# Kernel optimization log

Hardware: AMD Instinct MI355X
Metric: run time of the kernel (lower is better)

The kernel has to match this reference:

```python
import jax, jax.numpy as jnp
import numpy as np

B, LQ, LK, C = 16, 1024, 1024, 512
WH = int(LQ ** 0.5)  # 32


def setup_inputs() -> dict:
    key = jax.random.key(0)
    ks = jax.random.split(key, 6)
    s1 = 1.0 / np.sqrt(LK)
    return {
        "query": jax.random.normal(ks[0], (B, LQ, C), jnp.float32),
        "key": jax.random.normal(ks[1], (B, LK, C), jnp.float32),
        "value": jax.random.normal(ks[2], (B, LK, C), jnp.float32),
        # nn.Linear weights, stored [out_features, in_features] like torch
        "w1": jax.random.normal(ks[3], (LK, LK), jnp.float32) * s1,
        "w2": jax.random.normal(ks[4], (LK, LK), jnp.float32) * s1,
        "w3": jax.random.normal(ks[5], (1, LK), jnp.float32) * s1,
    }


def reference(query, key, value, w1, w2, w3):
    # cosine-similarity matrix (computed under no_grad in the original)
    q = query / 100.0
    k = key / 100.0
    qn = jnp.sqrt(jnp.sum(q * q, axis=-1))[:, :, None]   # [B, LQ, 1]
    kn = jnp.sqrt(jnp.sum(k * k, axis=-1))[:, None, :]   # [B, 1, LK]
    outer = qn * kn                                       # rank-1 outer product [B, LQ, LK]
    upper = jnp.einsum('bqc,bkc->bqk', q, k)              # [B, LQ, LK]
    similar_rev = jax.lax.stop_gradient(upper / (outer + 1e-6))

    # 3-layer MLP gating over the LK axis -> scalar weight per query row
    h = jax.nn.gelu(jnp.einsum('bqk,ok->bqo', similar_rev, w1), approximate=False)
    h = jax.nn.gelu(jnp.einsum('bqk,ok->bqo', h, w2), approximate=False)
    w = jnp.einsum('bqk,ok->bqo', h, w3)[..., 0]          # [B, LQ]

    # weight^T @ similar_rev / wh, then tanh -> per-key scalar gate [B, LK, 1]
    weight = jnp.einsum('bq,bqk->bk', w, similar_rev) / WH
    weight = jnp.tanh(weight)[:, :, None]

    # value modulation + residual
    return value * weight + value
```

## Files before the change

kernel.cpp:

```cpp
#include <hip/hip_runtime.h>
#include <hip/hip_bf16.h>

#define B_  16
#define LQ_ 1024
#define LK_ 1024
#define C_  512

typedef __attribute__((ext_vector_type(4))) float f32x4;
typedef __attribute__((ext_vector_type(8))) short bf16x8;

__device__ __forceinline__ float bf2f(ushort u) {
  union { unsigned int i; float f; } v; v.i = ((unsigned int)u) << 16; return v.f;
}
__device__ __forceinline__ ushort f2bf(float f) {
  union { float f; unsigned int i; } v; v.f = f;
  unsigned int r = v.i + 0x7fffu + ((v.i >> 16) & 1u);
  return (ushort)(r >> 16);
}
__device__ __forceinline__ float gelu_fast(float x) {
  float u = x * (0.7978845608f + 0.0356774081f * x * x);
  u = fminf(fmaxf(u, -9.f), 9.f);
  float e = __expf(2.f * u);
  float t = (e - 1.f) / (e + 1.f);
  return 0.5f * x * (1.f + t);
}

__device__ __forceinline__ void gload_lds16(const ushort* g, ushort* l) {
  __builtin_amdgcn_global_load_lds(
      (const __attribute__((address_space(1))) void*)g,
      (__attribute__((address_space(3))) void*)l, 16, 0, 0);
}

__global__ __launch_bounds__(256) void prep_all(
    const float* __restrict__ q, const float* __restrict__ k,
    const float* __restrict__ w1, const float* __restrict__ w2,
    ushort* __restrict__ Qb, ushort* __restrict__ Kb,
    ushort* __restrict__ W1b, ushort* __restrict__ W2b,
    float* __restrict__ qn, float* __restrict__ kn) {
  int wid = blockIdx.x * 4 + (threadIdx.x >> 6);
  int lane = threadIdx.x & 63;
  const float* src;
  ushort* dst;
  float* nrm = nullptr;
  if (wid < 16384) {
    src = q + (long)wid * C_;  dst = Qb + (long)wid * C_;  nrm = qn + wid;
  } else if (wid < 32768) {
    int r = wid - 16384;
    src = k + (long)r * C_;    dst = Kb + (long)r * C_;    nrm = kn + r;
  } else if (wid < 34816) {
    int r = wid - 32768;
    src = w1 + (long)r * C_;   dst = W1b + (long)r * C_;
  } else {
    int r = wid - 34816;
    src = w2 + (long)r * C_;   dst = W2b + (long)r * C_;
  }
  float ss = 0.f;
#pragma unroll
  for (int i0 = 0; i0 < 2; ++i0) {
    int i = lane * 4 + i0 * 256;
    float4 v = *(const float4*)(src + i);
    ss += v.x * v.x + v.y * v.y + v.z * v.z + v.w * v.w;
    ushort4 o;
    o.x = f2bf(v.x); o.y = f2bf(v.y); o.z = f2bf(v.z); o.w = f2bf(v.w);
    *(ushort4*)(dst + i) = o;
  }
  if (nrm) {
#pragma unroll
    for (int off = 32; off > 0; off >>= 1) ss += __shfl_xor(ss, off);
    if (lane == 0) *nrm = sqrtf(ss);
  }
}

#define BK 32

template <int EPI>
__device__ __forceinline__ void gemm128_body(
    const ushort* __restrict__ A, const ushort* __restrict__ Bm,
    ushort* __restrict__ Cc, int K, long sA, long sB, long sC,
    const float* __restrict__ qn, const float* __restrict__ kn,
    const float* __restrict__ w3v, float* __restrict__ wv) {
  int per = (int)(gridDim.x >> 3);
  int orig = blockIdx.x;
  int id = (orig & 7) * per + (orig >> 3);
  int b = id >> 6;
  int rtile = id & 63;
  const int bm = (rtile >> 3) * 128, bn = (rtile & 7) * 128;

  A += (long)b * sA;
  Bm += (long)b * sB;

  __shared__ ushort smem[16384];

  int tid = threadIdx.x;
  int lane = tid & 63, w = tid >> 6;
  int wr = w >> 1, wc = w & 1;
  int l16 = lane & 15, lhi = lane >> 4;

  f32x4 acc[4][4] = {};

  int c0 = tid, c1 = tid + 256;
  int r0 = c0 >> 2, cb0 = (c0 & 3) ^ ((r0 >> 1) & 3);
  int r1 = c1 >> 2, cb1 = (c1 & 3) ^ ((r1 >> 1) & 3);
  int wb0 = (tid & ~63) * 8;
  int wb1 = wb0 + 256 * 8;

  const ushort* Ar0 = A + (long)(bm + r0) * K + cb0 * 8;
  const ushort* Ar1 = A + (long)(bm + r1) * K + cb1 * 8;
  const ushort* Br0 = Bm + (long)(bn + r0) * K + cb0 * 8;
  const ushort* Br1 = Bm + (long)(bn + r1) * K + cb1 * 8;

  const int nt = K / BK;
  gload_lds16(Ar0, smem + wb0);
  gload_lds16(Ar1, smem + wb1);
  gload_lds16(Br0, smem + 8192 + wb0);
  gload_lds16(Br1, smem + 8192 + wb1);
  __syncthreads();

  int cur = 0;
  for (int t = 0; t < nt; ++t) {
    if (t + 1 < nt) {
      int k1 = (t + 1) * BK;
      int nx = (cur ^ 1) * 4096;
      gload_lds16(Ar0 + k1, smem + nx + wb0);
      gload_lds16(Ar1 + k1, smem + nx + wb1);
      gload_lds16(Br0 + k1, smem + 8192 + nx + wb0);
      gload_lds16(Br1 + k1, smem + 8192 + nx + wb1);
    }

    const ushort* Ac = smem + cur * 4096;
    const ushort* Bc = smem + 8192 + cur * 4096;
    bf16x8 af[4], bfr[4];
#pragma unroll
    for (int m = 0; m < 4; ++m) {
      int r = wr * 64 + m * 16 + l16;
      af[m] = *(const bf16x8*)(Ac + r * 32 + ((lhi ^ ((r >> 1) & 3)) * 8));
    }
#pragma unroll
    for (int n = 0; n < 4; ++n) {
      int r = wc * 64 + n * 16 + l16;
      bfr[n] = *(const bf16x8*)(Bc + r * 32 + ((lhi ^ ((r >> 1) & 3)) * 8));
    }
#pragma unroll
    for (int m = 0; m < 4; ++m)
#pragma unroll
      for (int n = 0; n < 4; ++n)
        acc[m][n] = __builtin_amdgcn_mfma_f32_16x16x32_bf16(af[m], bfr[n],
                                                            acc[m][n], 0, 0, 0);
    __syncthreads();
    cur ^= 1;
  }

  if constexpr (EPI == 2) {
    float* wvb = wv + (long)b * LQ_;
    float w3c[4];
#pragma unroll
    for (int n = 0; n < 4; ++n) w3c[n] = w3v[bn + wc * 64 + n * 16 + l16];
#pragma unroll
    for (int m = 0; m < 4; ++m)
#pragma unroll
      for (int rr = 0; rr < 4; ++rr) {
        float s = 0.f;
#pragma unroll
        for (int n = 0; n < 4; ++n)
          s += gelu_fast(acc[m][n][rr]) * w3c[n];
        s += __shfl_xor(s, 1);
        s += __shfl_xor(s, 2);
        s += __shfl_xor(s, 4);
        s += __shfl_xor(s, 8);
        if (l16 == 0)
          atomicAdd(&wvb[bm + wr * 64 + m * 16 + lhi * 4 + rr], s);
      }
  } else {
    Cc += (long)b * sC;
    const float* qnb = qn + (long)b * LQ_;
    const float* knb = kn + (long)b * LK_;
#pragma unroll
    for (int m = 0; m < 4; ++m) {
      int row0 = bm + wr * 64 + m * 16 + lhi * 4;
#pragma unroll
      for (int n = 0; n < 4; ++n) {
        int col = bn + wc * 64 + n * 16 + l16;
#pragma unroll
        for (int rr = 0; rr < 4; ++rr) {
          float v = acc[m][n][rr];
          int grow = row0 + rr;
          if (EPI == 0) {
            v = v / (qnb[grow] * knb[col] + 1e-2f);
          } else {
            v = gelu_fast(v);
          }
          Cc[(long)grow * 1024 + col] = f2bf(v);
        }
      }
    }
  }
}

__global__ __launch_bounds__(256, 2) void gemm_s(
    const ushort* __restrict__ A, const ushort* __restrict__ Bm,
    ushort* __restrict__ Cc, const float* __restrict__ qn,
    const float* __restrict__ kn) {
  gemm128_body<0>(A, Bm, Cc, C_, (long)LQ_ * C_, (long)LK_ * C_,
                  (long)LQ_ * LK_, qn, kn, nullptr, nullptr);
}

__global__ __launch_bounds__(256, 2) void gemm_h1(
    const ushort* __restrict__ A, const ushort* __restrict__ Bm,
    ushort* __restrict__ Cc) {
  gemm128_body<1>(A, Bm, Cc, LK_, (long)LQ_ * LK_, 0L, (long)LQ_ * LK_,
                  nullptr, nullptr, nullptr, nullptr);
}

__global__ __launch_bounds__(256, 2) void gemm_h2w(
    const ushort* __restrict__ A, const ushort* __restrict__ Bm,
    const float* __restrict__ w3v, float* __restrict__ wv) {
  gemm128_body<2>(A, Bm, nullptr, LK_, (long)LQ_ * LK_, 0L, 0L,
                  nullptr, nullptr, w3v, wv);
}

__global__ __launch_bounds__(256) void gate_partial(const ushort* __restrict__ S,
                                                    const float* __restrict__ wv,
                                                    float* __restrict__ wraw) {
  int b = blockIdx.z;
  int q0 = blockIdx.y * 64;
  int k4 = threadIdx.x * 4;
  const ushort* p = S + (long)b * LQ_ * LK_ + (long)q0 * LK_ + k4;
  const float* wb = wv + b * LQ_ + q0;
  float a0 = 0.f, a1 = 0.f, a2 = 0.f, a3 = 0.f;
#pragma unroll 4
  for (int q = 0; q < 64; ++q) {
    float wq = wb[q];
    ushort4 s4 = *(const ushort4*)(p + (long)q * LK_);
    a0 += wq * bf2f(s4.x);
    a1 += wq * bf2f(s4.y);
    a2 += wq * bf2f(s4.z);
    a3 += wq * bf2f(s4.w);
  }
  float* wr = wraw + b * LK_ + k4;
  atomicAdd(wr + 0, a0);
  atomicAdd(wr + 1, a1);
  atomicAdd(wr + 2, a2);
  atomicAdd(wr + 3, a3);
}

__global__ __launch_bounds__(256) void finalize(const float* __restrict__ value,
                                                const float* __restrict__ wraw,
                                                float* __restrict__ out) {
  long i = (long)blockIdx.x * 256 + threadIdx.x;
  long e = i * 4;
  int row = (int)(e >> 9);
  float g = 1.f + tanhf(wraw[row] * (1.f / 32.f));
  float4 v = ((const float4*)value)[i];
  v.x *= g; v.y *= g; v.z *= g; v.w *= g;
  ((float4*)out)[i] = v;
}

extern "C" void kernel_launch(void* const* d_in, const int* in_sizes, int n_in,
                              void* d_out, int out_size, void* d_ws,
                              size_t ws_size, hipStream_t stream) {
  const float* query = (const float*)d_in[0];
  const float* key   = (const float*)d_in[1];
  const float* value = (const float*)d_in[2];
  const float* w1    = (const float*)d_in[3];
  const float* w2    = (const float*)d_in[4];
  const float* w3    = (const float*)d_in[5];
  float* out = (float*)d_out;

  const size_t QB_BYTES = (size_t)B_ * LQ_ * C_ * 2;
  const size_t S_BYTES  = (size_t)B_ * LQ_ * LK_ * 2;
  const size_t W_BYTES  = (size_t)LK_ * LK_ * 2;
  const size_t OFF_QB = 0;
  const size_t OFF_KB = OFF_QB + QB_BYTES;
  const size_t OFF_S  = OFF_KB + QB_BYTES;
  const size_t OFF_H1 = OFF_S + S_BYTES;
  const size_t OFF_W1 = OFF_H1 + S_BYTES;
  const size_t OFF_W2 = OFF_W1 + W_BYTES;
  const size_t OFF_QN = OFF_W2 + W_BYTES;
  const size_t OFF_KN = OFF_QN + (size_t)B_ * LQ_ * 4;
  const size_t OFF_WV = OFF_KN + (size_t)B_ * LK_ * 4;
  const size_t OFF_WR = OFF_WV + (size_t)B_ * LQ_ * 4;
  const size_t TOTAL  = OFF_WR + (size_t)B_ * LK_ * 4;
  if (ws_size < TOTAL) return;

  char* ws = (char*)d_ws;
  ushort* Qb  = (ushort*)(ws + OFF_QB);
  ushort* Kb  = (ushort*)(ws + OFF_KB);
  ushort* S   = (ushort*)(ws + OFF_S);
  ushort* h1  = (ushort*)(ws + OFF_H1);
  ushort* W1b = (ushort*)(ws + OFF_W1);
  ushort* W2b = (ushort*)(ws + OFF_W2);
  float* qn   = (float*)(ws + OFF_QN);
  float* kn   = (float*)(ws + OFF_KN);
  float* wv   = (float*)(ws + OFF_WV);
  float* wraw = (float*)(ws + OFF_WR);

  prep_all<<<dim3(9216), 256, 0, stream>>>(query, key, w1, w2, Qb, Kb, W1b,
                                           W2b, qn, kn);
  hipMemsetAsync(wraw, 0, (size_t)B_ * LK_ * 4, stream);
  hipMemsetAsync(wv, 0, (size_t)B_ * LQ_ * 4, stream);

  gemm_s<<<dim3(1024), 256, 0, stream>>>(Qb, Kb, S, qn, kn);

  gemm_h1<<<dim3(1024), 256, 0, stream>>>(S, W1b, h1);

  gemm_h2w<<<dim3(1024), 256, 0, stream>>>(h1, W2b, w3, wv);

  gate_partial<<<dim3(1, 16, B_), 256, 0, stream>>>(S, wv, wraw);

  finalize<<<dim3((size_t)B_ * LK_ * C_ / 4 / 256), 256, 0, stream>>>(value, wraw, out);
}
```

Before: 171.3 us.

## Switch all GEMM operands and intermediates from bf16 to fp8 e4m3 MFMA

```diff
diff --git a/kernel.cpp b/kernel.cpp
--- a/kernel.cpp
+++ b/kernel.cpp
@@ -7,15 +7,10 @@
 #define C_  512
 
 typedef __attribute__((ext_vector_type(4))) float f32x4;
-typedef __attribute__((ext_vector_type(8))) short bf16x8;
+typedef unsigned char uchar;
 
 __device__ __forceinline__ float bf2f(ushort u) {
   union { unsigned int i; float f; } v; v.i = ((unsigned int)u) << 16; return v.f;
-}
-__device__ __forceinline__ ushort f2bf(float f) {
-  union { float f; unsigned int i; } v; v.f = f;
-  unsigned int r = v.i + 0x7fffu + ((v.i >> 16) & 1u);
-  return (ushort)(r >> 16);
 }
 __device__ __forceinline__ float gelu_fast(float x) {
   float u = x * (0.7978845608f + 0.0356774081f * x * x);
@@ -25,7 +20,31 @@
   return 0.5f * x * (1.f + t);
 }
 
-__device__ __forceinline__ void gload_lds16(const ushort* g, ushort* l) {
+__device__ __forceinline__ uchar f2fp8(float x) {
+  float ax = fabsf(x);
+  ax = fminf(ax, 448.f);
+  unsigned int sgn = (__float_as_uint(x) >> 24) & 0x80u;
+  unsigned int b;
+  if (ax >= 0.015625f) {
+    unsigned int u = __float_as_uint(ax);
+    u += 0x7FFFFu + ((u >> 20) & 1u);
+    unsigned int e = (u >> 23) - 120u;
+    b = (e << 3) | ((u >> 20) & 7u);
+  } else {
+    b = (unsigned int)(ax * 512.f + 0.5f);
+  }
+  return (uchar)(sgn | b);
+}
+__device__ __forceinline__ float fp82f(unsigned int b) {
+  unsigned int e = (b >> 3) & 15u, m = b & 7u;
+  unsigned int ee = e ? e : 1u;
+  unsigned int mm = m + (e ? 8u : 0u);
+  union { unsigned int u; float f; } p; p.u = (ee + 117u) << 23;
+  float r = (float)mm * p.f;
+  return (b & 0x80u) ? -r : r;
+}
+
+__device__ __forceinline__ void gload_lds16(const uchar* g, uchar* l) {
   __builtin_amdgcn_global_load_lds(
       (const __attribute__((address_space(1))) void*)g,
       (__attribute__((address_space(3))) void*)l, 16, 0, 0);
@@ -34,14 +53,15 @@
 __global__ __launch_bounds__(256) void prep_all(
     const float* __restrict__ q, const float* __restrict__ k,
     const float* __restrict__ w1, const float* __restrict__ w2,
-    ushort* __restrict__ Qb, ushort* __restrict__ Kb,
-    ushort* __restrict__ W1b, ushort* __restrict__ W2b,
+    uchar* __restrict__ Qb, uchar* __restrict__ Kb,
+    uchar* __restrict__ W1b, uchar* __restrict__ W2b,
     float* __restrict__ qn, float* __restrict__ kn) {
   int wid = blockIdx.x * 4 + (threadIdx.x >> 6);
   int lane = threadIdx.x & 63;
   const float* src;
-  ushort* dst;
+  uchar* dst;
   float* nrm = nullptr;
+  float scale = 1.f;
   if (wid < 16384) {
     src = q + (long)wid * C_;  dst = Qb + (long)wid * C_;  nrm = qn + wid;
   } else if (wid < 32768) {
@@ -49,10 +69,10 @@
     src = k + (long)r * C_;    dst = Kb + (long)r * C_;    nrm = kn + r;
   } else if (wid < 34816) {
     int r = wid - 32768;
-    src = w1 + (long)r * C_;   dst = W1b + (long)r * C_;
+    src = w1 + (long)r * C_;   dst = W1b + (long)r * C_;   scale = 32.f;
   } else {
     int r = wid - 34816;
-    src = w2 + (long)r * C_;   dst = W2b + (long)r * C_;
+    src = w2 + (long)r * C_;   dst = W2b + (long)r * C_;   scale = 32.f;
   }
   float ss = 0.f;
 #pragma unroll
@@ -60,9 +80,11 @@
     int i = lane * 4 + i0 * 256;
     float4 v = *(const float4*)(src + i);
     ss += v.x * v.x + v.y * v.y + v.z * v.z + v.w * v.w;
-    ushort4 o;
-    o.x = f2bf(v.x); o.y = f2bf(v.y); o.z = f2bf(v.z); o.w = f2bf(v.w);
-    *(ushort4*)(dst + i) = o;
+    unsigned int pk = (unsigned int)f2fp8(v.x * scale) |
+                      ((unsigned int)f2fp8(v.y * scale) << 8) |
+                      ((unsigned int)f2fp8(v.z * scale) << 16) |
+                      ((unsigned int)f2fp8(v.w * scale) << 24);
+    *(unsigned int*)(dst + i) = pk;
   }
   if (nrm) {
 #pragma unroll
@@ -75,8 +97,8 @@
 
 template <int EPI>
 __device__ __forceinline__ void gemm128_body(
-    const ushort* __restrict__ A, const ushort* __restrict__ Bm,
-    ushort* __restrict__ Cc, int K, long sA, long sB, long sC,
+    const uchar* __restrict__ A, const uchar* __restrict__ Bm,
+    uchar* __restrict__ Cc, int K, long sA, long sB, long sC,
     const float* __restrict__ qn, const float* __restrict__ kn,
     const float* __restrict__ w3v, float* __restrict__ wv) {
   int per = (int)(gridDim.x >> 3);
@@ -89,7 +111,7 @@
   A += (long)b * sA;
   Bm += (long)b * sB;
 
-  __shared__ ushort smem[16384];
+  __shared__ uchar smem[16384];
 
   int tid = threadIdx.x;
   int lane = tid & 63, w = tid >> 6;
@@ -98,22 +120,16 @@
 
   f32x4 acc[4][4] = {};
 
-  int c0 = tid, c1 = tid + 256;
-  int r0 = c0 >> 2, cb0 = (c0 & 3) ^ ((r0 >> 1) & 3);
-  int r1 = c1 >> 2, cb1 = (c1 & 3) ^ ((r1 >> 1) & 3);
-  int wb0 = (tid & ~63) * 8;
-  int wb1 = wb0 + 256 * 8;
-
-  const ushort* Ar0 = A + (long)(bm + r0) * K + cb0 * 8;
-  const ushort* Ar1 = A + (long)(bm + r1) * K + cb1 * 8;
-  const ushort* Br0 = Bm + (long)(bn + r0) * K + cb0 * 8;
-  const ushort* Br1 = Bm + (long)(bn + r1) * K + cb1 * 8;
+  int sr = tid >> 1;
+  int sh = (tid & 1) ^ (sr & 1);
+  int wb = (tid & ~63) * 16;
+
+  const uchar* Asrc = A + (long)(bm + sr) * K + sh * 16;
+  const uchar* Bsrc = Bm + (long)(bn + sr) * K + sh * 16;
 
   const int nt = K / BK;
-  gload_lds16(Ar0, smem + wb0);
-  gload_lds16(Ar1, smem + wb1);
-  gload_lds16(Br0, smem + 8192 + wb0);
-  gload_lds16(Br1, smem + 8192 + wb1);
+  gload_lds16(Asrc, smem + wb);
+  gload_lds16(Bsrc, smem + 8192 + wb);
   __syncthreads();
 
   int cur = 0;
@@ -121,31 +137,29 @@
     if (t + 1 < nt) {
       int k1 = (t + 1) * BK;
       int nx = (cur ^ 1) * 4096;
-      gload_lds16(Ar0 + k1, smem + nx + wb0);
-      gload_lds16(Ar1 + k1, smem + nx + wb1);
-      gload_lds16(Br0 + k1, smem + 8192 + nx + wb0);
-      gload_lds16(Br1 + k1, smem + 8192 + nx + wb1);
+      gload_lds16(Asrc + k1, smem + nx + wb);
+      gload_lds16(Bsrc + k1, smem + 8192 + nx + wb);
     }
 
-    const ushort* Ac = smem + cur * 4096;
-    const ushort* Bc = smem + 8192 + cur * 4096;
-    bf16x8 af[4], bfr[4];
+    const uchar* Ac = smem + cur * 4096;
+    const uchar* Bc = smem + 8192 + cur * 4096;
+    long af[4], bfr[4];
 #pragma unroll
     for (int m = 0; m < 4; ++m) {
       int r = wr * 64 + m * 16 + l16;
-      af[m] = *(const bf16x8*)(Ac + r * 32 + ((lhi ^ ((r >> 1) & 3)) * 8));
+      af[m] = *(const long*)(Ac + r * 32 + (((lhi >> 1) ^ (r & 1)) * 16 + (lhi & 1) * 8));
     }
 #pragma unroll
     for (int n = 0; n < 4; ++n) {
       int r = wc * 64 + n * 16 + l16;
-      bfr[n] = *(const bf16x8*)(Bc + r * 32 + ((lhi ^ ((r >> 1) & 3)) * 8));
+      bfr[n] = *(const long*)(Bc + r * 32 + (((lhi >> 1) ^ (r & 1)) * 16 + (lhi & 1) * 8));
     }
 #pragma unroll
     for (int m = 0; m < 4; ++m)
 #pragma unroll
       for (int n = 0; n < 4; ++n)
-        acc[m][n] = __builtin_amdgcn_mfma_f32_16x16x32_bf16(af[m], bfr[n],
-                                                            acc[m][n], 0, 0, 0);
+        acc[m][n] = __builtin_amdgcn_mfma_f32_16x16x32_fp8_fp8(
+            af[m], bfr[n], acc[m][n], 0, 0, 0);
     __syncthreads();
     cur ^= 1;
   }
@@ -162,7 +176,7 @@
         float s = 0.f;
 #pragma unroll
         for (int n = 0; n < 4; ++n)
-          s += gelu_fast(acc[m][n][rr]) * w3c[n];
+          s += gelu_fast(acc[m][n][rr] * (1.f / 512.f)) * w3c[n];
         s += __shfl_xor(s, 1);
         s += __shfl_xor(s, 2);
         s += __shfl_xor(s, 4);
@@ -187,9 +201,9 @@
           if (EPI == 0) {
             v = v / (qnb[grow] * knb[col] + 1e-2f);
           } else {
-            v = gelu_fast(v);
+            v = gelu_fast(v * (1.f / 512.f));
           }
-          Cc[(long)grow * 1024 + col] = f2bf(v);
+          Cc[(long)grow * 1024 + col] = f2fp8(v * 16.f);
         }
       }
     }
@@ -197,44 +211,44 @@
 }
 
 __global__ __launch_bounds__(256, 2) void gemm_s(
-    const ushort* __restrict__ A, const ushort* __restrict__ Bm,
-    ushort* __restrict__ Cc, const float* __restrict__ qn,
+    const uchar* __restrict__ A, const uchar* __restrict__ Bm,
+    uchar* __restrict__ Cc, const float* __restrict__ qn,
     const float* __restrict__ kn) {
   gemm128_body<0>(A, Bm, Cc, C_, (long)LQ_ * C_, (long)LK_ * C_,
                   (long)LQ_ * LK_, qn, kn, nullptr, nullptr);
 }
 
 __global__ __launch_bounds__(256, 2) void gemm_h1(
-    const ushort* __restrict__ A, const ushort* __restrict__ Bm,
-    ushort* __restrict__ Cc) {
+    const uchar* __restrict__ A, const uchar* __restrict__ Bm,
+    uchar* __restrict__ Cc) {
   gemm128_body<1>(A, Bm, Cc, LK_, (long)LQ_ * LK_, 0L, (long)LQ_ * LK_,
                   nullptr, nullptr, nullptr, nullptr);
 }
 
 __global__ __launch_bounds__(256, 2) void gemm_h2w(
-    const ushort* __restrict__ A, const ushort* __restrict__ Bm,
+    const uchar* __restrict__ A, const uchar* __restrict__ Bm,
     const float* __restrict__ w3v, float* __restrict__ wv) {
   gemm128_body<2>(A, Bm, nullptr, LK_, (long)LQ_ * LK_, 0L, 0L,
                   nullptr, nullptr, w3v, wv);
 }
 
-__global__ __launch_bounds__(256) void gate_partial(const ushort* __restrict__ S,
+__global__ __launch_bounds__(256) void gate_partial(const uchar* __restrict__ S,
                                                     const float* __restrict__ wv,
                                                     float* __restrict__ wraw) {
   int b = blockIdx.z;
   int q0 = blockIdx.y * 64;
   int k4 = threadIdx.x * 4;
-  const ushort* p = S + (long)b * LQ_ * LK_ + (long)q0 * LK_ + k4;
+  const uchar* p = S + (long)b * LQ_ * LK_ + (long)q0 * LK_ + k4;
   const float* wb = wv + b * LQ_ + q0;
   float a0 = 0.f, a1 = 0.f, a2 = 0.f, a3 = 0.f;
 #pragma unroll 4
   for (int q = 0; q < 64; ++q) {
     float wq = wb[q];
-    ushort4 s4 = *(const ushort4*)(p + (long)q * LK_);
-    a0 += wq * bf2f(s4.x);
-    a1 += wq * bf2f(s4.y);
-    a2 += wq * bf2f(s4.z);
-    a3 += wq * bf2f(s4.w);
+    unsigned int s4 = *(const unsigned int*)(p + (long)q * LK_);
+    a0 += wq * fp82f(s4 & 0xFF);
+    a1 += wq * fp82f((s4 >> 8) & 0xFF);
+    a2 += wq * fp82f((s4 >> 16) & 0xFF);
+    a3 += wq * fp82f(s4 >> 24);
   }
   float* wr = wraw + b * LK_ + k4;
   atomicAdd(wr + 0, a0);
@@ -249,7 +263,7 @@
   long i = (long)blockIdx.x * 256 + threadIdx.x;
   long e = i * 4;
   int row = (int)(e >> 9);
-  float g = 1.f + tanhf(wraw[row] * (1.f / 32.f));
+  float g = 1.f + tanhf(wraw[row] * (1.f / 512.f));
   float4 v = ((const float4*)value)[i];
   v.x *= g; v.y *= g; v.z *= g; v.w *= g;
   ((float4*)out)[i] = v;
@@ -266,9 +280,9 @@
   const float* w3    = (const float*)d_in[5];
   float* out = (float*)d_out;
 
-  const size_t QB_BYTES = (size_t)B_ * LQ_ * C_ * 2;
-  const size_t S_BYTES  = (size_t)B_ * LQ_ * LK_ * 2;
-  const size_t W_BYTES  = (size_t)LK_ * LK_ * 2;
+  const size_t QB_BYTES = (size_t)B_ * LQ_ * C_;
+  const size_t S_BYTES  = (size_t)B_ * LQ_ * LK_;
+  const size_t W_BYTES  = (size_t)LK_ * LK_;
   const size_t OFF_QB = 0;
   const size_t OFF_KB = OFF_QB + QB_BYTES;
   const size_t OFF_S  = OFF_KB + QB_BYTES;
@@ -283,12 +297,12 @@
   if (ws_size < TOTAL) return;
 
   char* ws = (char*)d_ws;
-  ushort* Qb  = (ushort*)(ws + OFF_QB);
-  ushort* Kb  = (ushort*)(ws + OFF_KB);
-  ushort* S   = (ushort*)(ws + OFF_S);
-  ushort* h1  = (ushort*)(ws + OFF_H1);
-  ushort* W1b = (ushort*)(ws + OFF_W1);
-  ushort* W2b = (ushort*)(ws + OFF_W2);
+  uchar* Qb  = (uchar*)(ws + OFF_QB);
+  uchar* Kb  = (uchar*)(ws + OFF_KB);
+  uchar* S   = (uchar*)(ws + OFF_S);
+  uchar* h1  = (uchar*)(ws + OFF_H1);
+  uchar* W1b = (uchar*)(ws + OFF_W1);
+  uchar* W2b = (uchar*)(ws + OFF_W2);
   float* qn   = (float*)(ws + OFF_QN);
   float* kn   = (float*)(ws + OFF_KN);
   float* wv   = (float*)(ws + OFF_WV);
```

Result: faster. 166.7 us (-2.7%).
